# Optimization experiments

Measured on AMD Instinct MI355X. Metric: run time of the kernel, lower is better.

The kernel has to match this reference:

```python
import jax, jax.numpy as jnp
import numpy as np

B, N, M, C = 8, 4096, 4096, 256
KS = 5          # dwc kernel size
FOCUS = 3.0     # focusing factor
EPS = 1e-6


def setup_inputs() -> dict:
    key = jax.random.key(0)
    ks = jax.random.split(key, 12)
    inp = {
        'query': jax.random.normal(ks[0], (B, N, C), jnp.float32),
        'key':   jax.random.normal(ks[1], (B, M, C), jnp.float32),
        'value': jax.random.normal(ks[2], (B, M, C), jnp.float32),
        'Wq':    jax.random.normal(ks[3], (C, C), jnp.float32) * 0.02,
        'Wk':    jax.random.normal(ks[4], (C, C), jnp.float32) * 0.02,
        'Wv':    jax.random.normal(ks[5], (C, C), jnp.float32) * 0.02,
        'Wproj': jax.random.normal(ks[6], (C, C), jnp.float32) * 0.02,
        'bproj': jax.random.normal(ks[7], (C,), jnp.float32) * 0.02,
        'dwc_w': jax.random.normal(ks[8], (C, 1, KS, KS), jnp.float32) * 0.02,
        'dwc_b': jax.random.normal(ks[9], (C,), jnp.float32) * 0.02,
        'scale': jax.random.normal(ks[10], (1, 1, C), jnp.float32) * 0.02,
        'H': 64,
        'W': 64,
    }
    return inp


def _dwconv(x, w, b):
    # x: (B, C, H, W), depthwise conv, SAME padding
    pad = KS // 2
    y = jax.lax.conv_general_dilated(
        x, w, window_strides=(1, 1), padding=[(pad, pad), (pad, pad)],
        dimension_numbers=('NCHW', 'OIHW', 'NCHW'), feature_group_count=C)
    return y + b[None, :, None, None]


def reference(query, key, value, Wq, Wk, Wv, Wproj, bproj, dwc_w, dwc_b, scale, H, W):
    q = jnp.einsum('bnc,dc->bnd', query, Wq)
    k = jnp.einsum('bmc,dc->bmd', key, Wk)
    v = jnp.einsum('bmc,dc->bmd', value, Wv)

    sc = jax.nn.softplus(scale)  # (1,1,C)
    q = (jax.nn.relu(q) + EPS) / sc
    k = (jax.nn.relu(k) + EPS) / sc

    q_norm = jnp.linalg.norm(q, axis=-1, keepdims=True)
    k_norm = jnp.linalg.norm(k, axis=-1, keepdims=True)
    # faithful to source: power then divide/multiply by the pre-power norm
    q = q ** FOCUS / q_norm * q_norm
    k = k ** FOCUS / k_norm * k_norm

    k_sum = k.sum(axis=1)                                   # (B, C)
    z_num = jnp.einsum('bnc,bc->bn', q, k_sum)              # (B, N)
    z = 1.0 / (z_num + EPS)

    kv = jnp.einsum('bmc,bmd->bcd', k, v)                   # (B, C, C)
    x = jnp.einsum('bnc,bcd->bnd', q, kv) * z[:, :, None]   # (B, N, C)

    xmap = x.transpose(0, 2, 1).reshape(x.shape[0], C, H, W)
    xmap = _dwconv(xmap, dwc_w, dwc_b)
    x = xmap.reshape(x.shape[0], C, H * W).transpose(0, 2, 1)

    x = x + q
    x = jnp.einsum('bnc,dc->bnd', x, Wproj) + bproj
    return x
```

## Files before the change

### kernel.cpp

```cpp
#include <hip/hip_runtime.h>
#include <math.h>
#include <stdint.h>

#define EPSF 1e-6f

typedef _Float16 half_t;
typedef _Float16 half8 __attribute__((ext_vector_type(8)));
typedef _Float16 half4 __attribute__((ext_vector_type(4)));
typedef float f32x4 __attribute__((ext_vector_type(4)));

#define MFMA16(A, B, C) __builtin_amdgcn_mfma_f32_16x16x32_f16(A, B, C, 0, 0, 0)

__device__ __forceinline__ float softplusf(float x) {
  return (x > 20.f) ? x : log1pf(expf(x));
}

__device__ __forceinline__ void split4(const float4 v, half4& h, half4& l) {
  h.x = (half_t)v.x; l.x = (half_t)(v.x - (float)h.x);
  h.y = (half_t)v.y; l.y = (half_t)(v.y - (float)h.y);
  h.z = (half_t)v.z; l.z = (half_t)(v.z - (float)h.z);
  h.w = (half_t)v.w; l.w = (half_t)(v.w - (float)h.w);
}


__device__ __forceinline__ void stage_gld(const half_t* __restrict__ src, size_t rowbase,
                                          int ld, int k0, half_t* __restrict__ dst, int tid) {
#pragma unroll
  for (int r = 0; r < 2; ++r) {
    const int f = tid + r * 256;
    const half_t* g = src + (rowbase + (size_t)(f >> 2)) * (size_t)ld + k0 + (f & 3) * 8;
    const __attribute__((address_space(1))) unsigned int* gp =
        (const __attribute__((address_space(1))) unsigned int*)(uintptr_t)g;
    __attribute__((address_space(3))) unsigned int* lp =
        (__attribute__((address_space(3))) unsigned int*)(uintptr_t)(dst + f * 8);
    __builtin_amdgcn_global_load_lds(gp, lp, 16, 0, 0);
  }
}

__device__ __forceinline__ void frag_compute(const half_t* __restrict__ As_h,
                                             const half_t* __restrict__ As_l,
                                             const half_t* __restrict__ Bs_h,
                                             const half_t* __restrict__ Bs_l,
                                             f32x4 (&acc)[4][4], int lane, int wm, int wn) {
  const int lr = lane & 15, lg = lane >> 4;
  half8 ah[4], al[4], bh[4], bl[4];
#pragma unroll
  for (int i = 0; i < 4; ++i) {
    const int ar = (wm * 64 + i * 16 + lr) * 32 + lg * 8;
    ah[i] = *(const half8*)&As_h[ar];
    al[i] = *(const half8*)&As_l[ar];
    const int br = (wn * 64 + i * 16 + lr) * 32 + lg * 8;
    bh[i] = *(const half8*)&Bs_h[br];
    bl[i] = *(const half8*)&Bs_l[br];
  }
#pragma unroll
  for (int i = 0; i < 4; ++i)
#pragma unroll
    for (int j = 0; j < 4; ++j) {
      acc[i][j] = MFMA16(ah[i], bh[j], acc[i][j]);
      acc[i][j] = MFMA16(ah[i], bl[j], acc[i][j]);
      acc[i][j] = MFMA16(al[i], bh[j], acc[i][j]);
    }
}

__global__ void scale_prep(const float* __restrict__ scale, float* __restrict__ scs) {
  const int c = threadIdx.x;
  scs[c] = 1.f / softplusf(scale[c]);
}

__global__ __launch_bounds__(256) void proj_mfma(
    const float* __restrict__ query, const float* __restrict__ key,
    const float* __restrict__ value,
    const float* __restrict__ Wq, const float* __restrict__ Wk, const float* __restrict__ Wv,
    const float* __restrict__ rsc,
    half_t* __restrict__ qh, half_t* __restrict__ ql,
    half_t* __restrict__ khT, half_t* __restrict__ klT,
    half_t* __restrict__ vhT, half_t* __restrict__ vlT) {
  const int which = blockIdx.z;
  const int tid = threadIdx.x;
  const int lane = tid & 63, wave = tid >> 6, wm = wave >> 1, wn = wave & 1;
  const int lr = lane & 15, lg = lane >> 4;

  const float* srcA;
  const float* srcB;
  int rA0, rB0;
  if (which == 0) {
    srcA = Wq;    rA0 = blockIdx.y * 128;  srcB = query; rB0 = blockIdx.x * 128;
  } else if (which == 1) {
    srcA = key;   rA0 = blockIdx.x * 128;  srcB = Wk;    rB0 = blockIdx.y * 128;
  } else {
    srcA = value; rA0 = blockIdx.x * 128;  srcB = Wv;    rB0 = blockIdx.y * 128;
  }

  __shared__ __align__(16) half_t sm[32768];
  f32x4 acc[4][4] = {};
  float4 RA[2][4], RB[2][4];

  auto load_tile = [&](float4 (&ra)[4], float4 (&rb)[4], int ks) {
    const int k0 = ks * 32;
#pragma unroll
    for (int r = 0; r < 4; ++r) {
      const int f = tid + r * 256;
      const int row = f >> 3, c4 = f & 7;
      ra[r] = *(const float4*)&srcA[(size_t)(rA0 + row) * 256 + k0 + c4 * 4];
      rb[r] = *(const float4*)&srcB[(size_t)(rB0 + row) * 256 + k0 + c4 * 4];
    }
  };
  auto split_write = [&](const float4 (&ra)[4], const float4 (&rb)[4], half_t* base) {
#pragma unroll
    for (int r = 0; r < 4; ++r) {
      const int f = tid + r * 256;
      const int row = f >> 3, c4 = f & 7;
      half4 h, l;
      split4(ra[r], h, l);
      *(half4*)&base[row * 32 + c4 * 4] = h;
      *(half4*)&base[4096 + row * 32 + c4 * 4] = l;
      split4(rb[r], h, l);
      *(half4*)&base[8192 + row * 32 + c4 * 4] = h;
      *(half4*)&base[12288 + row * 32 + c4 * 4] = l;
    }
  };

  load_tile(RA[0], RB[0], 0);
  split_write(RA[0], RB[0], sm);
  load_tile(RA[1], RB[1], 1);
  __syncthreads();
#pragma unroll
  for (int t = 0; t < 8; ++t) {
    if (t + 2 < 8) load_tile(RA[t & 1], RB[t & 1], t + 2);
    half_t* base = sm + (t & 1) * 16384;
    frag_compute(base, base + 4096, base + 8192, base + 12288, acc, lane, wm, wn);
    if (t + 1 < 8) split_write(RA[(t + 1) & 1], RB[(t + 1) & 1], sm + ((t + 1) & 1) * 16384);
    __syncthreads();
  }

  if (which == 0) {
    const int dbase = rA0 + wm * 64;
    float rs[4][4];
#pragma unroll
    for (int i = 0; i < 4; ++i)
#pragma unroll
      for (int r = 0; r < 4; ++r) rs[i][r] = rsc[dbase + i * 16 + lg * 4 + r];
#pragma unroll
    for (int j = 0; j < 4; ++j) {
      const size_t nflat = (size_t)rB0 + wn * 64 + j * 16 + lr;
#pragma unroll
      for (int i = 0; i < 4; ++i) {
        half4 hv, lv;
#pragma unroll
        for (int r = 0; r < 4; ++r) {
          float v = acc[i][j][r];
          v = (fmaxf(v, 0.f) + EPSF) * rs[i][r];
          v = v * v * v;
          const half_t h = (half_t)v;
          hv[r] = h;
          lv[r] = (half_t)(v - (float)h);
        }
        const size_t o = nflat * 256 + dbase + i * 16 + lg * 4;
        *(half4*)&qh[o] = hv;
        *(half4*)&ql[o] = lv;
      }
    }
  } else {
    const int b = rA0 >> 12, m0 = rA0 & 4095;
    half_t* Thg = (which == 1) ? khT : vhT;
    half_t* Tlg = (which == 1) ? klT : vlT;
    const bool act = (which == 1);
    half_t* Tt = sm;
    half_t* Tl2 = sm + 4352;
#pragma unroll
    for (int g = 0; g < 4; ++g) {
      if (wn == (g >> 1)) {
#pragma unroll
        for (int jj = 0; jj < 2; ++jj) {
          const int j = (g & 1) * 2 + jj;
          const int c = rB0 + wn * 64 + j * 16 + lr;
          const float rv = act ? rsc[c] : 1.f;
          const int crel = jj * 16 + lr;
#pragma unroll
          for (int i = 0; i < 4; ++i) {
            const int ml = wm * 64 + i * 16 + lg * 4;
            half4 hv, lv;
#pragma unroll
            for (int r = 0; r < 4; ++r) {
              float v = acc[i][j][r];
              if (act) { v = (fmaxf(v, 0.f) + EPSF) * rv; v = v * v * v; }
              const half_t h = (half_t)v;
              hv[r] = h;
              lv[r] = (half_t)(v - (float)h);
            }
            *(half4*)&Tt[crel * 136 + ml] = hv;
            *(half4*)&Tl2[crel * 136 + ml] = lv;
          }
        }
      }
      __syncthreads();
      {
        const int cr = tid >> 3, mm = (tid & 7) * 16;
        const size_t ga = ((size_t)(b * 256 + rB0 + g * 32 + cr)) * 4096 + m0 + mm;
        *(half8*)&Thg[ga]     = *(const half8*)&Tt[cr * 136 + mm];
        *(half8*)&Thg[ga + 8] = *(const half8*)&Tt[cr * 136 + mm + 8];
        *(half8*)&Tlg[ga]     = *(const half8*)&Tl2[cr * 136 + mm];
        *(half8*)&Tlg[ga + 8] = *(const half8*)&Tl2[cr * 136 + mm + 8];
      }
      __syncthreads();
    }
  }
}

__global__ __launch_bounds__(256) void ksum_k(const half_t* __restrict__ khT,
                                              const half_t* __restrict__ klT,
                                              float* __restrict__ ksm) {
  const int bc = blockIdx.x;
  const size_t base = (size_t)bc * 4096 + threadIdx.x * 16;
  float s = 0.f;
#pragma unroll
  for (int p = 0; p < 2; ++p) {
    const half8 h = *(const half8*)&khT[base + p * 8];
    const half8 l = *(const half8*)&klT[base + p * 8];
#pragma unroll
    for (int u = 0; u < 8; ++u) s += (float)h[u] + (float)l[u];
  }
  __shared__ float rbuf[256];
  rbuf[threadIdx.x] = s;
  __syncthreads();
  for (int off = 128; off > 0; off >>= 1) {
    if (threadIdx.x < off) rbuf[threadIdx.x] += rbuf[threadIdx.x + off];
    __syncthreads();
  }
  if (threadIdx.x == 0) ksm[bc] = rbuf[0];
}

__global__ __launch_bounds__(256) void kv_mfma(
    const half_t* __restrict__ vhT, const half_t* __restrict__ vlT,
    const half_t* __restrict__ khT, const half_t* __restrict__ klT,
    float* __restrict__ kvp) {
  const int b = blockIdx.z >> 3, s = blockIdx.z & 7;
  const int d0 = blockIdx.x * 128, c0 = blockIdx.y * 128;
  const int tid = threadIdx.x;
  __shared__ __align__(16) half_t sm[32768];
  f32x4 acc[4][4] = {};
  const int lane = tid & 63, wave = tid >> 6, wm = wave >> 1, wn = wave & 1;
  const int lr = lane & 15, lg = lane >> 4;
  const size_t arow = (size_t)b * 256 + d0, brow = (size_t)b * 256 + c0;

  auto stage = [&](int bi, int ks) {
    half_t* base = sm + bi * 16384;
    const int k0 = s * 512 + ks * 32;
    stage_gld(vhT, arow, 4096, k0, base, tid);
    stage_gld(vlT, arow, 4096, k0, base + 4096, tid);
    stage_gld(khT, brow, 4096, k0, base + 8192, tid);
    stage_gld(klT, brow, 4096, k0, base + 12288, tid);
  };

  stage(0, 0);
  __syncthreads();
  for (int t = 0; t < 16; ++t) {
    if (t + 1 < 16) stage((t + 1) & 1, t + 1);
    half_t* base = sm + (t & 1) * 16384;
    frag_compute(base, base + 4096, base + 8192, base + 12288, acc, lane, wm, wn);
    __syncthreads();
  }

  float* outp = kvp + ((size_t)(b * 8 + s)) * 65536;
#pragma unroll
  for (int j = 0; j < 4; ++j) {
    const int c = c0 + wn * 64 + j * 16 + lr;
#pragma unroll
    for (int i = 0; i < 4; ++i) {
      const int d = d0 + wm * 64 + i * 16 + lg * 4;
#pragma unroll
      for (int r = 0; r < 4; ++r) outp[(size_t)(d + r) * 256 + c] = acc[i][j][r];
    }
  }
}

__global__ __launch_bounds__(256) void kv_red(const float* __restrict__ kvp,
                                              half_t* __restrict__ kvTh,
                                              half_t* __restrict__ kvTl) {
  const size_t idx = (size_t)blockIdx.x * 256 + threadIdx.x;
  const int b = (int)(idx >> 16);
  const int dc = (int)(idx & 65535);
  float s = 0.f;
#pragma unroll
  for (int t = 0; t < 8; ++t) s += kvp[((size_t)(b * 8 + t)) * 65536 + dc];
  const half_t h = (half_t)s;
  kvTh[idx] = h;
  kvTl[idx] = (half_t)(s - (float)h);
}

__global__ __launch_bounds__(256) void z_k(const half_t* __restrict__ qh,
                                           const half_t* __restrict__ ql,
                                           const float* __restrict__ ksm,
                                           float* __restrict__ zb) {
  const int wid = threadIdx.x >> 6, lane = threadIdx.x & 63;
  const int row = blockIdx.x * 4 + wid;
  const int b = row >> 12;
  const half4 h = *(const half4*)&qh[(size_t)row * 256 + lane * 4];
  const half4 l = *(const half4*)&ql[(size_t)row * 256 + lane * 4];
  const float4 kc = *(const float4*)&ksm[b * 256 + lane * 4];
  float d = ((float)h[0] + (float)l[0]) * kc.x + ((float)h[1] + (float)l[1]) * kc.y +
            ((float)h[2] + (float)l[2]) * kc.z + ((float)h[3] + (float)l[3]) * kc.w;
#pragma unroll
  for (int off = 32; off > 0; off >>= 1) d += __shfl_xor(d, off, 64);
  if (lane == 0) zb[row] = 1.f / (d + EPSF);
}

__global__ __launch_bounds__(256) void x1_mfma(
    const half_t* __restrict__ qh, const half_t* __restrict__ ql,
    const half_t* __restrict__ kvTh, const half_t* __restrict__ kvTl,
    const float* __restrict__ zb, float* __restrict__ xt) {
  const int b = blockIdx.z, n0 = blockIdx.x * 128, d0t = blockIdx.y * 128;
  const int tid = threadIdx.x;
  __shared__ __align__(16) half_t sm[32768];
  f32x4 acc[4][4] = {};
  const int lane = tid & 63, wave = tid >> 6, wm = wave >> 1, wn = wave & 1;
  const int lr = lane & 15, lg = lane >> 4;
  const size_t arow = (size_t)b * 4096 + n0, brow = (size_t)b * 256 + d0t;

  auto stage = [&](int bi, int ks) {
    half_t* base = sm + bi * 16384;
    const int k0 = ks * 32;
    stage_gld(qh, arow, 256, k0, base, tid);
    stage_gld(ql, arow, 256, k0, base + 4096, tid);
    stage_gld(kvTh, brow, 256, k0, base + 8192, tid);
    stage_gld(kvTl, brow, 256, k0, base + 12288, tid);
  };

  stage(0, 0);
  __syncthreads();
  for (int t = 0; t < 8; ++t) {
    if (t + 1 < 8) stage((t + 1) & 1, t + 1);
    half_t* base = sm + (t & 1) * 16384;
    frag_compute(base, base + 4096, base + 8192, base + 12288, acc, lane, wm, wn);
    __syncthreads();
  }

#pragma unroll
  for (int i = 0; i < 4; ++i) {
    const int nb = n0 + wm * 64 + i * 16 + lg * 4;
    float zr[4];
#pragma unroll
    for (int r = 0; r < 4; ++r) zr[r] = zb[b * 4096 + nb + r];
#pragma unroll
    for (int j = 0; j < 4; ++j) {
      const int d = d0t + wn * 64 + j * 16 + lr;
      *(float4*)&xt[((size_t)b * 256 + d) * 4096 + nb] =
          make_float4(acc[i][j][0] * zr[0], acc[i][j][1] * zr[1],
                      acc[i][j][2] * zr[2], acc[i][j][3] * zr[3]);
    }
  }
}

__global__ __launch_bounds__(256) void dwconv_kernel(const float* __restrict__ xt,
                                                     const float* __restrict__ w,
                                                     const float* __restrict__ bias,
                                                     float* __restrict__ xc) {
  const int bc = blockIdx.x;
  const int c = bc & 255;
  const float* plane = xt + (size_t)bc * 4096;
  float* oplane = xc + (size_t)bc * 4096;

  __shared__ float Ls[68][72];
  const int tid = threadIdx.x;
  for (int i = tid; i < 68 * 72; i += 256) ((float*)Ls)[i] = 0.f;
  __syncthreads();
#pragma unroll
  for (int p = 0; p < 4; ++p) {
    const int f = tid + p * 256;
    const int y = f >> 4, x4 = f & 15;
    *(float4*)&Ls[2 + y][4 + x4 * 4] = *(const float4*)&plane[y * 64 + x4 * 4];
  }
  __syncthreads();

  float wreg[25];
#pragma unroll
  for (int t = 0; t < 25; ++t) wreg[t] = w[c * 25 + t];
  const float bv = bias[c];

  const int x = tid & 63, ys0 = (tid >> 6) * 16;
  float win[5][5];
#pragma unroll
  for (int r = 0; r < 5; ++r)
#pragma unroll
    for (int cx = 0; cx < 5; ++cx) win[r][cx] = Ls[ys0 + r][x + 2 + cx];

  for (int yy = 0; yy < 16; ++yy) {
    float s = bv;
#pragma unroll
    for (int ky = 0; ky < 5; ++ky)
#pragma unroll
      for (int kx = 0; kx < 5; ++kx) s = fmaf(win[ky][kx], wreg[ky * 5 + kx], s);
    oplane[(ys0 + yy) * 64 + x] = s;
    if (yy < 15) {
#pragma unroll
      for (int r = 0; r < 4; ++r)
#pragma unroll
        for (int cx = 0; cx < 5; ++cx) win[r][cx] = win[r + 1][cx];
#pragma unroll
      for (int cx = 0; cx < 5; ++cx) win[4][cx] = Ls[ys0 + yy + 5][x + 2 + cx];
    }
  }
}

__global__ __launch_bounds__(256) void final_mfma(
    const half_t* __restrict__ qh, const half_t* __restrict__ ql,
    const float* __restrict__ xc, const float* __restrict__ Wp,
    const float* __restrict__ bp, float* __restrict__ outp) {
  const int b = blockIdx.z, n0 = blockIdx.x * 128, dd0 = blockIdx.y * 128;
  const int tid = threadIdx.x;
  __shared__ __align__(16) half_t As_h[4096], As_l[4096], Bs_h[4096], Bs_l[4096];
  __shared__ __align__(16) float Xs[32 * 130];
  f32x4 acc[4][4] = {};
  const int lane = tid & 63, wave = tid >> 6, wm = wave >> 1, wn = wave & 1;
  const int lr = lane & 15, lg = lane >> 4;

  float4 rxs[4], rwp[4];
  half8 rqh[2][2], rql[2][2];

  auto load_xw = [&](int ks) {
    const int k0 = ks * 32;
#pragma unroll
    for (int r = 0; r < 4; ++r) {
      const int f = tid + r * 256;
      rxs[r] = *(const float4*)&xc[((size_t)b * 256 + k0 + (f >> 5)) * 4096 + n0 + (f & 31) * 4];
      rwp[r] = *(const float4*)&Wp[(size_t)(dd0 + (f >> 3)) * 256 + k0 + (f & 7) * 4];
    }
  };

  load_xw(0);
#pragma unroll
  for (int r = 0; r < 2; ++r) {
    const int f = tid + r * 256;
    const size_t qoff = ((size_t)b * 4096 + n0 + (f >> 2)) * 256 + (f & 3) * 8;
    rqh[0][r] = *(const half8*)&qh[qoff];
    rql[0][r] = *(const half8*)&ql[qoff];
  }

#pragma unroll
  for (int t = 0; t < 8; ++t) {
#pragma unroll
    for (int r = 0; r < 4; ++r) {
      const int f = tid + r * 256;
      const int cc = f >> 5, n4 = f & 31;
      *(float2*)&Xs[cc * 130 + n4 * 4] = make_float2(rxs[r].x, rxs[r].y);
      *(float2*)&Xs[cc * 130 + n4 * 4 + 2] = make_float2(rxs[r].z, rxs[r].w);
      half4 h, l;
      split4(rwp[r], h, l);
      *(half4*)&Bs_h[(f >> 3) * 32 + (f & 7) * 4] = h;
      *(half4*)&Bs_l[(f >> 3) * 32 + (f & 7) * 4] = l;
    }
    __syncthreads();
#pragma unroll
    for (int r = 0; r < 2; ++r) {
      const int f = tid + r * 256, row = f >> 2, ch = f & 3;
      const half8 h8 = rqh[t & 1][r];
      const half8 l8 = rql[t & 1][r];
      half8 oh, ol;
#pragma unroll
      for (int u = 0; u < 8; ++u) {
        const float v = (float)h8[u] + (float)l8[u] + Xs[(ch * 8 + u) * 130 + row];
        const half_t h = (half_t)v;
        oh[u] = h;
        ol[u] = (half_t)(v - (float)h);
      }
      *(half8*)&As_h[row * 32 + ch * 8] = oh;
      *(half8*)&As_l[row * 32 + ch * 8] = ol;
    }
    __syncthreads();
    if (t + 1 < 8) {
      load_xw(t + 1);
      const int k0n = (t + 1) * 32;
#pragma unroll
      for (int r = 0; r < 2; ++r) {
        const int f = tid + r * 256;
        const size_t qoff = ((size_t)b * 4096 + n0 + (f >> 2)) * 256 + k0n + (f & 3) * 8;
        rqh[(t + 1) & 1][r] = *(const half8*)&qh[qoff];
        rql[(t + 1) & 1][r] = *(const half8*)&ql[qoff];
      }
    }
    frag_compute(As_h, As_l, Bs_h, Bs_l, acc, lane, wm, wn);
    __syncthreads();
  }

#pragma unroll
  for (int j = 0; j < 4; ++j) {
    const int dd = dd0 + wn * 64 + j * 16 + lr;
    const float bb = bp[dd];
#pragma unroll
    for (int i = 0; i < 4; ++i) {
      const size_t rowg = (size_t)b * 4096 + n0 + wm * 64 + i * 16 + lg * 4;
#pragma unroll
      for (int r = 0; r < 4; ++r) outp[(rowg + r) * 256 + dd] = acc[i][j][r] + bb;
    }
  }
}

extern "C" void kernel_launch(void* const* d_in, const int* in_sizes, int n_in,
                              void* d_out, int out_size, void* d_ws, size_t ws_size,
                              hipStream_t stream) {
  const float* query = (const float*)d_in[0];
  const float* key   = (const float*)d_in[1];
  const float* value = (const float*)d_in[2];
  const float* Wq    = (const float*)d_in[3];
  const float* Wk    = (const float*)d_in[4];
  const float* Wv    = (const float*)d_in[5];
  const float* Wproj = (const float*)d_in[6];
  const float* bproj = (const float*)d_in[7];
  const float* dwc_w = (const float*)d_in[8];
  const float* dwc_b = (const float*)d_in[9];
  const float* scale = (const float*)d_in[10];

  const size_t U = (size_t)8 * 4096 * 256;
  half_t* qh  = (half_t*)d_ws;
  half_t* ql  = qh + U;
  half_t* khT = ql + U;
  half_t* klT = khT + U;
  half_t* vhT = klT + U;
  half_t* vlT = vhT + U;
  float*  kvp = (float*)(vlT + U);
  half_t* kvTh = (half_t*)(kvp + (size_t)8 * 8 * 65536);
  half_t* kvTl = kvTh + (size_t)8 * 65536;
  float*  ksm = (float*)(kvTl + (size_t)8 * 65536);
  float*  zbuf = ksm + 8 * 256;
  float*  scs  = zbuf + 32768;
  float* xt = (float*)khT;
  float* xc = (float*)vhT;
  float* outp = (float*)d_out;

  const dim3 blk(256);
  scale_prep<<<dim3(1), blk, 0, stream>>>(scale, scs);
  proj_mfma<<<dim3(256, 2, 3), blk, 0, stream>>>(query, key, value, Wq, Wk, Wv, scs,
                                                 qh, ql, khT, klT, vhT, vlT);
  ksum_k<<<dim3(2048), blk, 0, stream>>>(khT, klT, ksm);
  kv_mfma<<<dim3(2, 2, 64), blk, 0, stream>>>(vhT, vlT, khT, klT, kvp);
  kv_red<<<dim3(2048), blk, 0, stream>>>(kvp, kvTh, kvTl);
  z_k<<<dim3(8192), blk, 0, stream>>>(qh, ql, ksm, zbuf);
  x1_mfma<<<dim3(32, 2, 8), blk, 0, stream>>>(qh, ql, kvTh, kvTl, zbuf, xt);
  dwconv_kernel<<<dim3(2048), blk, 0, stream>>>(xt, dwc_w, dwc_b, xc);
  final_mfma<<<dim3(32, 2, 8), blk, 0, stream>>>(xc == nullptr ? qh : qh, ql, xc, Wproj, bproj, outp);
}
```

Baseline: 309.5 us.

## Fuse k-sum and z into GEMMs, triple-buffer staging, use lightweight barriers

The column sum of k is now accumulated in the projection epilogue through wave shuffles and atomics, which removes the separate ksum kernel. The z denominator is computed inside x1_mfma from the q tiles already staged in shared memory, which removes the z_k kernel and its extra read of q. kv_mfma and x1_mfma move from double to triple buffering, with explicit vmcnt/lgkmcnt waits and raw s_barrier in place of __syncthreads, so more loads stay in flight. Atomic summation makes the k-sum order nondeterministic, and the larger shared-memory footprint may lower occupancy.

```diff
diff --git a/kernel.cpp b/kernel.cpp
--- a/kernel.cpp
+++ b/kernel.cpp
@@ -10,6 +10,23 @@
 typedef float f32x4 __attribute__((ext_vector_type(4)));
 
 #define MFMA16(A, B, C) __builtin_amdgcn_mfma_f32_16x16x32_f16(A, B, C, 0, 0, 0)
+
+#define SBAR() __builtin_amdgcn_s_barrier()
+#define WAIT_LGKM0()                                        \
+  do {                                                      \
+    asm volatile("s_waitcnt lgkmcnt(0)" ::: "memory");      \
+    __builtin_amdgcn_sched_barrier(0);                      \
+  } while (0)
+#define WAIT_VM8_LGKM0()                                            \
+  do {                                                              \
+    asm volatile("s_waitcnt vmcnt(8) lgkmcnt(0)" ::: "memory");     \
+    __builtin_amdgcn_sched_barrier(0);                              \
+  } while (0)
+#define WAIT_VM0_LGKM0()                                            \
+  do {                                                              \
+    asm volatile("s_waitcnt vmcnt(0) lgkmcnt(0)" ::: "memory");     \
+    __builtin_amdgcn_sched_barrier(0);                              \
+  } while (0)
 
 __device__ __forceinline__ float softplusf(float x) {
   return (x > 20.f) ? x : log1pf(expf(x));
@@ -63,9 +80,11 @@
     }
 }
 
-__global__ void scale_prep(const float* __restrict__ scale, float* __restrict__ scs) {
-  const int c = threadIdx.x;
-  scs[c] = 1.f / softplusf(scale[c]);
+__global__ void init_k(const float* __restrict__ scale, float* __restrict__ scs,
+                       float* __restrict__ ksm) {
+  const int i = blockIdx.x * 256 + threadIdx.x;
+  if (i < 2048) ksm[i] = 0.f;
+  if (i < 256) scs[i] = 1.f / softplusf(scale[i]);
 }
 
 __global__ __launch_bounds__(256) void proj_mfma(
@@ -75,7 +94,8 @@
     const float* __restrict__ rsc,
     half_t* __restrict__ qh, half_t* __restrict__ ql,
     half_t* __restrict__ khT, half_t* __restrict__ klT,
-    half_t* __restrict__ vhT, half_t* __restrict__ vlT) {
+    half_t* __restrict__ vhT, half_t* __restrict__ vlT,
+    float* __restrict__ ksm) {
   const int which = blockIdx.z;
   const int tid = threadIdx.x;
   const int lane = tid & 63, wave = tid >> 6, wm = wave >> 1, wn = wave & 1;
@@ -124,14 +144,16 @@
   load_tile(RA[0], RB[0], 0);
   split_write(RA[0], RB[0], sm);
   load_tile(RA[1], RB[1], 1);
-  __syncthreads();
+  WAIT_LGKM0();
+  SBAR();
 #pragma unroll
   for (int t = 0; t < 8; ++t) {
     if (t + 2 < 8) load_tile(RA[t & 1], RB[t & 1], t + 2);
     half_t* base = sm + (t & 1) * 16384;
     frag_compute(base, base + 4096, base + 8192, base + 12288, acc, lane, wm, wn);
     if (t + 1 < 8) split_write(RA[(t + 1) & 1], RB[(t + 1) & 1], sm + ((t + 1) & 1) * 16384);
-    __syncthreads();
+    WAIT_LGKM0();
+    SBAR();
   }
 
   if (which == 0) {
@@ -168,6 +190,7 @@
     const bool act = (which == 1);
     half_t* Tt = sm;
     half_t* Tl2 = sm + 4352;
+    float kj[4] = {0.f, 0.f, 0.f, 0.f};
 #pragma unroll
     for (int g = 0; g < 4; ++g) {
       if (wn == (g >> 1)) {
@@ -184,7 +207,7 @@
 #pragma unroll
             for (int r = 0; r < 4; ++r) {
               float v = acc[i][j][r];
-              if (act) { v = (fmaxf(v, 0.f) + EPSF) * rv; v = v * v * v; }
+              if (act) { v = (fmaxf(v, 0.f) + EPSF) * rv; v = v * v * v; kj[j] += v; }
               const half_t h = (half_t)v;
               hv[r] = h;
               lv[r] = (half_t)(v - (float)h);
@@ -205,30 +228,16 @@
       }
       __syncthreads();
     }
-  }
-}
-
-__global__ __launch_bounds__(256) void ksum_k(const half_t* __restrict__ khT,
-                                              const half_t* __restrict__ klT,
-                                              float* __restrict__ ksm) {
-  const int bc = blockIdx.x;
-  const size_t base = (size_t)bc * 4096 + threadIdx.x * 16;
-  float s = 0.f;
-#pragma unroll
-  for (int p = 0; p < 2; ++p) {
-    const half8 h = *(const half8*)&khT[base + p * 8];
-    const half8 l = *(const half8*)&klT[base + p * 8];
-#pragma unroll
-    for (int u = 0; u < 8; ++u) s += (float)h[u] + (float)l[u];
-  }
-  __shared__ float rbuf[256];
-  rbuf[threadIdx.x] = s;
-  __syncthreads();
-  for (int off = 128; off > 0; off >>= 1) {
-    if (threadIdx.x < off) rbuf[threadIdx.x] += rbuf[threadIdx.x + off];
-    __syncthreads();
-  }
-  if (threadIdx.x == 0) ksm[bc] = rbuf[0];
+    if (act) {
+#pragma unroll
+      for (int j = 0; j < 4; ++j) {
+        float s = kj[j];
+        s += __shfl_xor(s, 16, 64);
+        s += __shfl_xor(s, 32, 64);
+        if (lg == 0) atomicAdd(&ksm[b * 256 + rB0 + wn * 64 + j * 16 + lr], s);
+      }
+    }
+  }
 }
 
 __global__ __launch_bounds__(256) void kv_mfma(
@@ -238,7 +247,7 @@
   const int b = blockIdx.z >> 3, s = blockIdx.z & 7;
   const int d0 = blockIdx.x * 128, c0 = blockIdx.y * 128;
   const int tid = threadIdx.x;
-  __shared__ __align__(16) half_t sm[32768];
+  __shared__ __align__(16) half_t sm[49152];
   f32x4 acc[4][4] = {};
   const int lane = tid & 63, wave = tid >> 6, wm = wave >> 1, wn = wave & 1;
   const int lr = lane & 15, lg = lane >> 4;
@@ -254,12 +263,16 @@
   };
 
   stage(0, 0);
-  __syncthreads();
+  stage(1, 1);
+  WAIT_VM8_LGKM0();
+  SBAR();
+#pragma unroll
   for (int t = 0; t < 16; ++t) {
-    if (t + 1 < 16) stage((t + 1) & 1, t + 1);
-    half_t* base = sm + (t & 1) * 16384;
+    if (t + 2 < 16) stage((t + 2) % 3, t + 2);
+    half_t* base = sm + (t % 3) * 16384;
     frag_compute(base, base + 4096, base + 8192, base + 12288, acc, lane, wm, wn);
-    __syncthreads();
+    if (t + 2 < 16) { WAIT_VM8_LGKM0(); } else { WAIT_VM0_LGKM0(); }
+    SBAR();
   }
 
   float* outp = kvp + ((size_t)(b * 8 + s)) * 65536;
@@ -289,30 +302,14 @@
   kvTl[idx] = (half_t)(s - (float)h);
 }
 
-__global__ __launch_bounds__(256) void z_k(const half_t* __restrict__ qh,
-                                           const half_t* __restrict__ ql,
-                                           const float* __restrict__ ksm,
-                                           float* __restrict__ zb) {
-  const int wid = threadIdx.x >> 6, lane = threadIdx.x & 63;
-  const int row = blockIdx.x * 4 + wid;
-  const int b = row >> 12;
-  const half4 h = *(const half4*)&qh[(size_t)row * 256 + lane * 4];
-  const half4 l = *(const half4*)&ql[(size_t)row * 256 + lane * 4];
-  const float4 kc = *(const float4*)&ksm[b * 256 + lane * 4];
-  float d = ((float)h[0] + (float)l[0]) * kc.x + ((float)h[1] + (float)l[1]) * kc.y +
-            ((float)h[2] + (float)l[2]) * kc.z + ((float)h[3] + (float)l[3]) * kc.w;
-#pragma unroll
-  for (int off = 32; off > 0; off >>= 1) d += __shfl_xor(d, off, 64);
-  if (lane == 0) zb[row] = 1.f / (d + EPSF);
-}
-
 __global__ __launch_bounds__(256) void x1_mfma(
     const half_t* __restrict__ qh, const half_t* __restrict__ ql,
     const half_t* __restrict__ kvTh, const half_t* __restrict__ kvTl,
-    const float* __restrict__ zb, float* __restrict__ xt) {
+    const float* __restrict__ ksm, float* __restrict__ xt) {
   const int b = blockIdx.z, n0 = blockIdx.x * 128, d0t = blockIdx.y * 128;
   const int tid = threadIdx.x;
-  __shared__ __align__(16) half_t sm[32768];
+  __shared__ __align__(16) half_t sm[49152];
+  __shared__ float zden[128];
   f32x4 acc[4][4] = {};
   const int lane = tid & 63, wave = tid >> 6, wm = wave >> 1, wn = wave & 1;
   const int lr = lane & 15, lg = lane >> 4;
@@ -328,24 +325,48 @@
   };
 
   stage(0, 0);
+  stage(1, 1);
+  WAIT_VM8_LGKM0();
+  SBAR();
+  float zpart = 0.f;
+  const int zrow = tid >> 1, zkh = tid & 1;
+#pragma unroll
+  for (int t = 0; t < 8; ++t) {
+    if (t + 2 < 8) stage((t + 2) % 3, t + 2);
+    half_t* base = sm + (t % 3) * 16384;
+    frag_compute(base, base + 4096, base + 8192, base + 12288, acc, lane, wm, wn);
+    {
+      const half_t* hp = base + zrow * 32 + zkh * 16;
+      const half_t* lp = base + 4096 + zrow * 32 + zkh * 16;
+      const half8 h0 = *(const half8*)&hp[0];
+      const half8 h1 = *(const half8*)&hp[8];
+      const half8 l0 = *(const half8*)&lp[0];
+      const half8 l1 = *(const half8*)&lp[8];
+      const float* ksp = ksm + b * 256 + t * 32 + zkh * 16;
+#pragma unroll
+      for (int u = 0; u < 8; ++u) {
+        zpart += ((float)h0[u] + (float)l0[u]) * ksp[u];
+        zpart += ((float)h1[u] + (float)l1[u]) * ksp[8 + u];
+      }
+    }
+    if (t + 2 < 8) { WAIT_VM8_LGKM0(); } else { WAIT_VM0_LGKM0(); }
+    SBAR();
+  }
+
+  zpart += __shfl_xor(zpart, 1, 64);
+  if ((tid & 1) == 0) zden[zrow] = zpart;
   __syncthreads();
-  for (int t = 0; t < 8; ++t) {
-    if (t + 1 < 8) stage((t + 1) & 1, t + 1);
-    half_t* base = sm + (t & 1) * 16384;
-    frag_compute(base, base + 4096, base + 8192, base + 12288, acc, lane, wm, wn);
-    __syncthreads();
-  }
 
 #pragma unroll
   for (int i = 0; i < 4; ++i) {
-    const int nb = n0 + wm * 64 + i * 16 + lg * 4;
+    const int nl = wm * 64 + i * 16 + lg * 4;
     float zr[4];
 #pragma unroll
-    for (int r = 0; r < 4; ++r) zr[r] = zb[b * 4096 + nb + r];
+    for (int r = 0; r < 4; ++r) zr[r] = 1.f / (zden[nl + r] + EPSF);
 #pragma unroll
     for (int j = 0; j < 4; ++j) {
       const int d = d0t + wn * 64 + j * 16 + lr;
-      *(float4*)&xt[((size_t)b * 256 + d) * 4096 + nb] =
+      *(float4*)&xt[((size_t)b * 256 + d) * 4096 + n0 + nl] =
           make_float4(acc[i][j][0] * zr[0], acc[i][j][1] * zr[1],
                       acc[i][j][2] * zr[2], acc[i][j][3] * zr[3]);
     }
@@ -450,7 +471,8 @@
       *(half4*)&Bs_h[(f >> 3) * 32 + (f & 7) * 4] = h;
       *(half4*)&Bs_l[(f >> 3) * 32 + (f & 7) * 4] = l;
     }
-    __syncthreads();
+    WAIT_LGKM0();
+    SBAR();
 #pragma unroll
     for (int r = 0; r < 2; ++r) {
       const int f = tid + r * 256, row = f >> 2, ch = f & 3;
@@ -467,7 +489,8 @@
       *(half8*)&As_h[row * 32 + ch * 8] = oh;
       *(half8*)&As_l[row * 32 + ch * 8] = ol;
     }
-    __syncthreads();
+    WAIT_LGKM0();
+    SBAR();
     if (t + 1 < 8) {
       load_xw(t + 1);
       const int k0n = (t + 1) * 32;
@@ -480,7 +503,8 @@
       }
     }
     frag_compute(As_h, As_l, Bs_h, Bs_l, acc, lane, wm, wn);
-    __syncthreads();
+    WAIT_LGKM0();
+    SBAR();
   }
 
 #pragma unroll
@@ -529,14 +553,12 @@
   float* outp = (float*)d_out;
 
   const dim3 blk(256);
-  scale_prep<<<dim3(1), blk, 0, stream>>>(scale, scs);
+  init_k<<<dim3(8), blk, 0, stream>>>(scale, scs, ksm);
   proj_mfma<<<dim3(256, 2, 3), blk, 0, stream>>>(query, key, value, Wq, Wk, Wv, scs,
-                                                 qh, ql, khT, klT, vhT, vlT);
-  ksum_k<<<dim3(2048), blk, 0, stream>>>(khT, klT, ksm);
+                                                 qh, ql, khT, klT, vhT, vlT, ksm);
   kv_mfma<<<dim3(2, 2, 64), blk, 0, stream>>>(vhT, vlT, khT, klT, kvp);
   kv_red<<<dim3(2048), blk, 0, stream>>>(kvp, kvTh, kvTl);
-  z_k<<<dim3(8192), blk, 0, stream>>>(qh, ql, ksm, zbuf);
-  x1_mfma<<<dim3(32, 2, 8), blk, 0, stream>>>(qh, ql, kvTh, kvTl, zbuf, xt);
+  x1_mfma<<<dim3(32, 2, 8), blk, 0, stream>>>(qh, ql, kvTh, kvTl, ksm, xt);
   dwconv_kernel<<<dim3(2048), blk, 0, stream>>>(xt, dwc_w, dwc_b, xc);
-  final_mfma<<<dim3(32, 2, 8), blk, 0, stream>>>(xc == nullptr ? qh : qh, ql, xc, Wproj, bproj, outp);
-}
+  final_mfma<<<dim3(32, 2, 8), blk, 0, stream>>>(qh, ql, xc, Wproj, bproj, outp);
+}
```

Result: faster. 300.4 us (-3.0%).
